# Kernel optimization log

Hardware: AMD Instinct MI355X
Metric: run time of the kernel (lower is better)

The kernel has to match this reference:

```python
import jax, jax.numpy as jnp
import numpy as np

LATENT_D = 32      # latent_dim
MAX_TRIES = 10     # max_tries_sampling
EPS = 1e-40

def _conv(x, W, b, stride, pad):
    y = jax.lax.conv_general_dilated(x, W, (stride, stride), [(pad, pad), (pad, pad)],
                                     dimension_numbers=('NCHW', 'OIHW', 'NCHW'))
    return y + b[None, :, None, None]

def _normalize(v, axis=-1):
    n = jnp.sqrt(jnp.clip(jnp.sum(v * v, axis=axis, keepdims=True), 1e-24))
    return v / n

def wood_sample_vMF(mu, kappa, key):
    # mu: [B,d] unit vectors, kappa: [B]
    B, d = mu.shape
    alpha = d - 1.0
    k_w, k_v = jax.random.split(key)

    def body(i, carry):
        w, acc = carry
        k1 = jax.random.fold_in(k_w, 2 * i)
        k2 = jax.random.fold_in(k_w, 2 * i + 1)
        w_cand = 2.0 * jax.random.uniform(k1, (B,)) - 1.0
        one_minus_w2 = jnp.clip(1.0 - w_cand * w_cand, EPS)
        log_p = kappa * w_cand + 0.5 * (alpha - 2.0) * jnp.log(one_minus_w2)
        log_r = jnp.log(jax.random.uniform(k2, (B,)) + EPS)
        newly = (log_r + kappa <= log_p) & (~acc)
        w = jnp.where(newly, w_cand, w)
        return w, acc | newly

    w, _ = jax.lax.fori_loop(0, MAX_TRIES, body,
                             (jnp.zeros((B,)), jnp.zeros((B,), dtype=bool)))
    w = jnp.clip(w, -1.0, 1.0)
    v = _normalize(jax.random.normal(k_v, (B, d - 1)))      # tangent direction
    sqrt_term = jnp.sqrt(jnp.clip(1.0 - w * w, EPS))
    z_tilde = jnp.concatenate([sqrt_term[:, None] * v, w[:, None]], axis=1)  # [B,d]
    e_d = jnp.zeros((d,)).at[-1].set(1.0)
    u = _normalize(e_d[None, :] - mu)                        # Householder axis
    dot_val = jnp.sum(z_tilde * u, axis=-1, keepdims=True)
    return z_tilde - 2.0 * dot_val * u

def setup_inputs() -> dict:
    key = jax.random.key(0)
    ks = jax.random.split(key, 16)
    B = 64
    s = 0.05
    inp = {
        'x':   jax.random.normal(ks[0], (B, 6, 224, 224), jnp.float32),
        # stand-in resnet encoder (resnet_out_dim=512)
        'W1':  jax.random.normal(ks[1], (64, 6, 7, 7)) * s,   'b1': jnp.zeros((64,)),
        'W2':  jax.random.normal(ks[2], (256, 64, 3, 3)) * s, 'b2': jnp.zeros((256,)),
        'Wh':  jax.random.normal(ks[3], (256, 512)) * s,      'bh': jnp.zeros((512,)),
        # vMF heads
        'Wmu': jax.random.normal(ks[4], (512, LATENT_D)) * s, 'bmu': jnp.zeros((LATENT_D,)),
        'Wk':  jax.random.normal(ks[5], (512, 1)) * s,        'bk': jnp.zeros((1,)),
        # ResNetMLP(32 -> 512 -> 512 -> 32 -> 7)
        'M1': jax.random.normal(ks[6], (LATENT_D, 512)) * s,  'bM1': jnp.zeros((512,)),
        'M2': jax.random.normal(ks[7], (512, 512)) * s,       'bM2': jnp.zeros((512,)),
        'M3': jax.random.normal(ks[8], (512, 32)) * s,        'bM3': jnp.zeros((32,)),
        'M4': jax.random.normal(ks[9], (32, 7)) * s,          'bM4': jnp.zeros((7,)),
    }
    return inp

def reference(x, W1, b1, W2, b2, Wh, bh, Wmu, bmu, Wk, bk,
              M1, bM1, M2, bM2, M3, bM3, M4, bM4):
    # encoder: conv stack -> global avg pool -> fc (resnet_out_dim=512)
    h = jax.nn.relu(_conv(x, W1, b1, stride=4, pad=3))   # [B,64,56,56]
    h = jax.nn.relu(_conv(h, W2, b2, stride=2, pad=1))   # [B,256,28,28]
    h = jnp.mean(h, axis=(2, 3))                         # [B,256]
    h = h @ Wh + bh                                      # [B,512]
    mu = _normalize(h @ Wmu + bmu)                       # [B,32] on sphere
    kappa = jax.nn.softplus(h @ Wk + bk) + 1.0           # [B,1]
    z = wood_sample_vMF(mu, kappa[:, 0], jax.random.key(42))
    # MLP head
    y = jax.nn.relu(z @ M1 + bM1)
    y = jax.nn.relu(y @ M2 + bM2)
    y = jax.nn.relu(y @ M3 + bM3)
    out = y @ M4 + bM4                                   # [B,7]
    return out, mu, kappa
```

## Files before the change

### kernel.cpp

```cpp
#include <hip/hip_runtime.h>
#include <hip/hip_bf16.h>
#include <cstdint>

__device__ __forceinline__ uint32_t rotl32(uint32_t v, int n) {
    return (v << n) | (v >> (32 - n));
}

__device__ __forceinline__ void threefry2x32(uint32_t k0, uint32_t k1,
                                             uint32_t x0, uint32_t x1,
                                             uint32_t& o0, uint32_t& o1) {
    uint32_t ks2 = 0x1BD11BDAu ^ k0 ^ k1;
    uint32_t v0 = x0 + k0, v1 = x1 + k1;
    v0 += v1; v1 = rotl32(v1, 13); v1 ^= v0;
    v0 += v1; v1 = rotl32(v1, 15); v1 ^= v0;
    v0 += v1; v1 = rotl32(v1, 26); v1 ^= v0;
    v0 += v1; v1 = rotl32(v1, 6);  v1 ^= v0;
    v0 += k1; v1 += ks2 + 1u;
    v0 += v1; v1 = rotl32(v1, 17); v1 ^= v0;
    v0 += v1; v1 = rotl32(v1, 29); v1 ^= v0;
    v0 += v1; v1 = rotl32(v1, 16); v1 ^= v0;
    v0 += v1; v1 = rotl32(v1, 24); v1 ^= v0;
    v0 += ks2; v1 += k0 + 2u;
    v0 += v1; v1 = rotl32(v1, 13); v1 ^= v0;
    v0 += v1; v1 = rotl32(v1, 15); v1 ^= v0;
    v0 += v1; v1 = rotl32(v1, 26); v1 ^= v0;
    v0 += v1; v1 = rotl32(v1, 6);  v1 ^= v0;
    v0 += k0; v1 += k1 + 3u;
    v0 += v1; v1 = rotl32(v1, 17); v1 ^= v0;
    v0 += v1; v1 = rotl32(v1, 29); v1 ^= v0;
    v0 += v1; v1 = rotl32(v1, 16); v1 ^= v0;
    v0 += v1; v1 = rotl32(v1, 24); v1 ^= v0;
    v0 += k1; v1 += ks2 + 4u;
    v0 += v1; v1 = rotl32(v1, 13); v1 ^= v0;
    v0 += v1; v1 = rotl32(v1, 15); v1 ^= v0;
    v0 += v1; v1 = rotl32(v1, 26); v1 ^= v0;
    v0 += v1; v1 = rotl32(v1, 6);  v1 ^= v0;
    v0 += ks2; v1 += k0 + 5u;
    o0 = v0; o1 = v1;
}

__device__ __forceinline__ float bits_to_unit_float(uint32_t bits) {
    return __uint_as_float((bits >> 9) | 0x3F800000u) - 1.0f;
}

__device__ __forceinline__ float erfinv_f(float x) {
    float w = -log1pf(-x * x);
    float p;
    if (w < 5.0f) {
        w = w - 2.5f;
        p = 2.81022636e-08f;
        p = fmaf(p, w, 3.43273939e-07f);
        p = fmaf(p, w, -3.5233877e-06f);
        p = fmaf(p, w, -4.39150654e-06f);
        p = fmaf(p, w, 0.00021858087f);
        p = fmaf(p, w, -0.00125372503f);
        p = fmaf(p, w, -0.00417768164f);
        p = fmaf(p, w, 0.246640727f);
        p = fmaf(p, w, 1.50140941f);
    } else {
        w = sqrtf(w) - 3.0f;
        p = -0.000200214257f;
        p = fmaf(p, w, 0.000100950558f);
        p = fmaf(p, w, 0.00134934322f);
        p = fmaf(p, w, -0.00367342844f);
        p = fmaf(p, w, 0.00573950773f);
        p = fmaf(p, w, -0.0076224613f);
        p = fmaf(p, w, 0.00943887047f);
        p = fmaf(p, w, 1.00167406f);
        p = fmaf(p, w, 2.83297682f);
    }
    return p * x;
}

__global__ __launch_bounds__(256) void transpose_W2(const float* __restrict__ W2,
                                                    float* __restrict__ W2T) {
    __shared__ float t[32][33];
    int pT = blockIdx.x % 18;
    int oT = blockIdx.x / 18;
    int c = threadIdx.x & 31, r8 = threadIdx.x >> 5;
    #pragma unroll
    for (int rr = 0; rr < 4; ++rr) {
        int oc = oT * 32 + r8 + 8 * rr;
        t[r8 + 8 * rr][c] = W2[oc * 576 + pT * 32 + c];
    }
    __syncthreads();
    #pragma unroll
    for (int rr = 0; rr < 4; ++rr) {
        int p = pT * 32 + r8 + 8 * rr;
        W2T[p * 256 + oT * 32 + c] = t[c][r8 + 8 * rr];
    }
}

__global__ __launch_bounds__(256) void conv1_tiled(const float* __restrict__ x,
                                                   const float* __restrict__ W1,
                                                   const float* __restrict__ b1,
                                                   float* __restrict__ out) {
    int bid = blockIdx.x;
    int ocT = bid & 1;
    int ohT = (bid >> 1) % 7;
    int b   = bid / 14;
    int tid = threadIdx.x;
    int ocg = tid & 3;
    int owg = (tid >> 2) & 7;
    int ohh = tid >> 5;

    __shared__ __align__(16) float w1s[294 * 32];
    for (int idx = tid; idx < 9408; idx += 256) {
        int p = idx >> 5, ocl = idx & 31;
        w1s[idx] = W1[(ocT * 32 + ocl) * 294 + p];
    }
    __syncthreads();

    int oh = ohT * 8 + ohh;
    int iwst = 28 * owg - 4;
    const float* xb = x + (size_t)b * 6 * 50176;

    float acc[8][7] = {};

    #pragma unroll 1
    for (int ic = 0; ic < 6; ++ic) {
        #pragma unroll 1
        for (int kh = 0; kh < 7; ++kh) {
            int ih = 4 * oh - 3 + kh;
            if ((unsigned)ih >= 224u) continue;
            const float* xrow = xb + ic * 50176 + ih * 224 + iwst;
            float r[32];
            {
                float2 v0 = (owg > 0) ? *reinterpret_cast<const float2*>(xrow)
                                      : make_float2(0.0f, 0.0f);
                float2 v1 = (owg > 0) ? *reinterpret_cast<const float2*>(xrow + 2)
                                      : make_float2(0.0f, 0.0f);
                r[0] = v0.x; r[1] = v0.y; r[2] = v1.x; r[3] = v1.y;
            }
            #pragma unroll
            for (int t = 2; t < 16; ++t) {
                float2 v2 = *reinterpret_cast<const float2*>(xrow + 2 * t);
                r[2 * t] = v2.x; r[2 * t + 1] = v2.y;
            }
            const float* wp = &w1s[(ic * 49 + kh * 7) * 32 + 8 * ocg];
            #pragma unroll
            for (int kw = 0; kw < 7; ++kw) {
                float4 wa = *reinterpret_cast<const float4*>(wp + kw * 32);
                float4 wb = *reinterpret_cast<const float4*>(wp + kw * 32 + 4);
                #pragma unroll
                for (int j = 0; j < 7; ++j) {
                    float xv = r[4 * j + kw + 1];
                    acc[0][j] = fmaf(xv, wa.x, acc[0][j]);
                    acc[1][j] = fmaf(xv, wa.y, acc[1][j]);
                    acc[2][j] = fmaf(xv, wa.z, acc[2][j]);
                    acc[3][j] = fmaf(xv, wa.w, acc[3][j]);
                    acc[4][j] = fmaf(xv, wb.x, acc[4][j]);
                    acc[5][j] = fmaf(xv, wb.y, acc[5][j]);
                    acc[6][j] = fmaf(xv, wb.z, acc[6][j]);
                    acc[7][j] = fmaf(xv, wb.w, acc[7][j]);
                }
            }
        }
    }

    int oc0 = ocT * 32 + 8 * ocg;
    #pragma unroll
    for (int q = 0; q < 8; ++q) {
        float bias = b1[oc0 + q];
        float* orow = out + (((size_t)b * 64 + oc0 + q) * 56 + oh) * 56 + 7 * owg;
        #pragma unroll
        for (int j = 0; j < 7; ++j) orow[j] = fmaxf(acc[q][j] + bias, 0.0f);
    }
}

__global__ __launch_bounds__(256) void conv2_tiled(const float* __restrict__ c1,
                                                   const float* __restrict__ W2T,
                                                   const float* __restrict__ b2,
                                                   float* __restrict__ part2) {
    int bid = blockIdx.x;
    int ocT = bid & 1;
    int ohT = (bid >> 1) % 7;
    int b   = bid / 14;
    int tid = threadIdx.x;
    int ocg = tid & 15;
    int owg = (tid >> 4) & 3;
    int ohh = tid >> 6;

    __shared__ __align__(16) float w2s[72 * 128];
    float* red = w2s;

    int oh = 4 * ohT + ohh;
    int start = 14 * owg - 2;

    float acc[8][7] = {};

    #pragma unroll 1
    for (int chunk = 0; chunk < 8; ++chunk) {
        int ic0 = chunk * 8;
        __syncthreads();
        for (int idx = tid; idx < 9216; idx += 256) {
            int pl = idx >> 7, ocl = idx & 127;
            w2s[idx] = W2T[((size_t)(ic0 * 9 + pl)) * 256 + ocT * 128 + ocl];
        }
        __syncthreads();

        #pragma unroll 1
        for (int icl = 0; icl < 8; ++icl) {
            const float* crow0 = c1 + (((size_t)b * 64 + ic0 + icl) * 56) * 56;
            #pragma unroll 1
            for (int kh = 0; kh < 3; ++kh) {
                int ih = 2 * oh - 1 + kh;
                if ((unsigned)ih >= 56u) continue;
                const float* xrow = crow0 + ih * 56 + start;
                float r[16];
                {
                    float2 v0 = (owg > 0) ? *reinterpret_cast<const float2*>(xrow)
                                          : make_float2(0.0f, 0.0f);
                    r[0] = v0.x; r[1] = v0.y;
                }
                #pragma unroll
                for (int t = 1; t < 8; ++t) {
                    float2 v2 = *reinterpret_cast<const float2*>(xrow + 2 * t);
                    r[2 * t] = v2.x; r[2 * t + 1] = v2.y;
                }
                int pb = icl * 9 + kh * 3;
                #pragma unroll
                for (int kw = 0; kw < 3; ++kw) {
                    float4 wa = *reinterpret_cast<const float4*>(&w2s[(pb + kw) * 128 + 4 * ocg]);
                    float4 wb = *reinterpret_cast<const float4*>(&w2s[(pb + kw) * 128 + 64 + 4 * ocg]);
                    #pragma unroll
                    for (int j = 0; j < 7; ++j) {
                        float xv = r[2 * j + kw + 1];
                        acc[0][j] = fmaf(xv, wa.x, acc[0][j]);
                        acc[1][j] = fmaf(xv, wa.y, acc[1][j]);
                        acc[2][j] = fmaf(xv, wa.z, acc[2][j]);
                        acc[3][j] = fmaf(xv, wa.w, acc[3][j]);
                        acc[4][j] = fmaf(xv, wb.x, acc[4][j]);
                        acc[5][j] = fmaf(xv, wb.y, acc[5][j]);
                        acc[6][j] = fmaf(xv, wb.z, acc[6][j]);
                        acc[7][j] = fmaf(xv, wb.w, acc[7][j]);
                    }
                }
            }
        }
    }

    __syncthreads();
    int sp = ohh * 4 + owg;
    #pragma unroll
    for (int q = 0; q < 8; ++q) {
        int ocl = (q < 4) ? (ocg * 4 + q) : (64 + ocg * 4 + (q - 4));
        float bias = b2[ocT * 128 + ocl];
        float s = 0.0f;
        #pragma unroll
        for (int j = 0; j < 7; ++j) s += fmaxf(acc[q][j] + bias, 0.0f);
        red[ocl * 16 + sp] = s;
    }
    __syncthreads();
    if (tid < 128) {
        float s = 0.0f;
        #pragma unroll
        for (int i = 0; i < 16; ++i) s += red[tid * 16 + i];
        part2[((size_t)ohT * 64 + b) * 256 + ocT * 128 + tid] = s;
    }
}

__global__ __launch_bounds__(512) void head_fused(const float* __restrict__ part2,
                                                  const float* __restrict__ Wh,
                                                  const float* __restrict__ bh,
                                                  const float* __restrict__ Wmu,
                                                  const float* __restrict__ bmu,
                                                  const float* __restrict__ Wk,
                                                  const float* __restrict__ bk,
                                                  float* __restrict__ out) {
    int b = blockIdx.x, tid = threadIdx.x;
    __shared__ float ps[256], hs[512], ms[32], red2[512], kred[16];
    __shared__ float nrm;
    if (tid < 256) {
        float s = 0.0f;
        #pragma unroll
        for (int t = 0; t < 7; ++t) s += part2[((size_t)t * 64 + b) * 256 + tid];
        ps[tid] = s * (1.0f / 784.0f);
    }
    __syncthreads();
    {
        float acc = bh[tid];
        for (int i = 0; i < 256; ++i) acc = fmaf(ps[i], Wh[i * 512 + tid], acc);
        hs[tid] = acc;
    }
    __syncthreads();
    {
        int m = tid >> 4, part = tid & 15;
        int j0 = part * 32;
        float acc = 0.0f;
        #pragma unroll
        for (int jj = 0; jj < 32; ++jj) acc = fmaf(hs[j0 + jj], Wmu[(j0 + jj) * 32 + m], acc);
        red2[m * 16 + part] = acc;
    }
    if (tid < 16) {
        int j0 = tid * 32;
        float acc = 0.0f;
        #pragma unroll
        for (int jj = 0; jj < 32; ++jj) acc = fmaf(hs[j0 + jj], Wk[j0 + jj], acc);
        kred[tid] = acc;
    }
    __syncthreads();
    if (tid < 32) {
        float acc = bmu[tid];
        #pragma unroll
        for (int p = 0; p < 16; ++p) acc += red2[tid * 16 + p];
        ms[tid] = acc;
    }
    if (tid == 32) {
        float acc = bk[0];
        #pragma unroll
        for (int p = 0; p < 16; ++p) acc += kred[p];
        float sp = fmaxf(acc, 0.0f) + log1pf(expf(-fabsf(acc)));
        out[2496 + b] = sp + 1.0f;
    }
    __syncthreads();
    if (tid == 0) {
        float ss = 0.0f;
        for (int k = 0; k < 32; ++k) ss += ms[k] * ms[k];
        nrm = sqrtf(fmaxf(ss, 1e-24f));
    }
    __syncthreads();
    if (tid < 32) out[448 + b * 32 + tid] = ms[tid] / nrm;
}

__global__ __launch_bounds__(512) void mlp_head(const float* __restrict__ M1, const float* __restrict__ bM1,
                                                const float* __restrict__ M2, const float* __restrict__ bM2,
                                                const float* __restrict__ M3, const float* __restrict__ bM3,
                                                const float* __restrict__ M4, const float* __restrict__ bM4,
                                                float* __restrict__ out) {
    int b = blockIdx.x;
    int tid = threadIdx.x;
    __shared__ float vsh[31], wcs[10], zsh[32], y1[512], y2[512], y3[32];
    __shared__ int accs[10];

    if (tid < 31) {
        uint32_t y00, y01, y10, y11;
        threefry2x32(0u, 42u, 0u, 2u, y00, y01);
        threefry2x32(0u, 42u, 1u, 3u, y10, y11);
        uint32_t kv0 = y01, kv1 = y11;
        int idx = b * 31 + tid;
        int word = (idx >= 992);
        uint32_t pp = (uint32_t)(word ? idx - 992 : idx);
        uint32_t a0, a1;
        threefry2x32(kv0, kv1, pp, 992u + pp, a0, a1);
        uint32_t bits = word ? a1 : a0;
        float f = bits_to_unit_float(bits);
        const float LO = -0.99999994f;
        float u = fmaxf(LO, f * 2.0f + LO);
        vsh[tid] = 1.41421356f * erfinv_f(u);
    } else if (tid >= 64 && tid < 74) {
        uint32_t y00, y01, y10, y11;
        threefry2x32(0u, 42u, 0u, 2u, y00, y01);
        threefry2x32(0u, 42u, 1u, 3u, y10, y11);
        uint32_t kw0 = y00, kw1 = y10;
        int i = tid - 64;
        float kappa = out[2496 + b];
        uint32_t k10, k11, k20, k21, z0, z1;
        threefry2x32(kw0, kw1, 0u, (uint32_t)(2 * i), k10, k11);
        threefry2x32(kw0, kw1, 0u, (uint32_t)(2 * i + 1), k20, k21);
        uint32_t p = (uint32_t)(b & 31);
        threefry2x32(k10, k11, p, 32u + p, z0, z1);
        uint32_t bits = (b < 32) ? z0 : z1;
        float u1 = bits_to_unit_float(bits);
        float wc = 2.0f * u1 - 1.0f;
        float om = fmaxf(1.0f - wc * wc, 1e-40f);
        float logp = kappa * wc + 14.5f * logf(om);
        threefry2x32(k20, k21, p, 32u + p, z0, z1);
        bits = (b < 32) ? z0 : z1;
        float logr = logf(bits_to_unit_float(bits) + 1e-40f);
        wcs[i] = wc;
        accs[i] = (logr + kappa <= logp) ? 1 : 0;
    }
    __syncthreads();
    if (tid == 0) {
        float w = 0.0f;
        bool acc = false;
        #pragma unroll
        for (int i = 0; i < 10; ++i) {
            bool newly = (accs[i] != 0) && !acc;
            if (newly) w = wcs[i];
            acc = acc || newly;
        }
        w = fminf(fmaxf(w, -1.0f), 1.0f);
        float ss = 0.0f;
        #pragma unroll
        for (int j = 0; j < 31; ++j) ss += vsh[j] * vsh[j];
        float vinv = 1.0f / sqrtf(fmaxf(ss, 1e-24f));
        float st = sqrtf(fmaxf(1.0f - w * w, 1e-40f));
        float zt[32];
        #pragma unroll
        for (int j = 0; j < 31; ++j) zt[j] = st * (vsh[j] * vinv);
        zt[31] = w;
        float uv[32];
        float us = 0.0f;
        #pragma unroll
        for (int k = 0; k < 32; ++k) {
            float m = out[448 + b * 32 + k];
            float e = (k == 31) ? 1.0f : 0.0f;
            float t = e - m;
            uv[k] = t;
            us += t * t;
        }
        float un = sqrtf(fmaxf(us, 1e-24f));
        float dot = 0.0f;
        #pragma unroll
        for (int k = 0; k < 32; ++k) {
            uv[k] = uv[k] / un;
            dot += zt[k] * uv[k];
        }
        #pragma unroll
        for (int k = 0; k < 32; ++k) zsh[k] = zt[k] - 2.0f * dot * uv[k];
    }
    __syncthreads();

    float acc = bM1[tid];
    #pragma unroll
    for (int k = 0; k < 32; k++) acc = fmaf(zsh[k], M1[k * 512 + tid], acc);
    y1[tid] = fmaxf(acc, 0.0f);
    __syncthreads();
    acc = bM2[tid];
    for (int k = 0; k < 512; k++) acc = fmaf(y1[k], M2[k * 512 + tid], acc);
    y2[tid] = fmaxf(acc, 0.0f);
    __syncthreads();
    if (tid < 32) {
        acc = bM3[tid];
        for (int k = 0; k < 512; k++) acc = fmaf(y2[k], M3[k * 32 + tid], acc);
        y3[tid] = fmaxf(acc, 0.0f);
    }
    __syncthreads();
    if (tid < 7) {
        acc = bM4[tid];
        #pragma unroll
        for (int k = 0; k < 32; k++) acc = fmaf(y3[k], M4[k * 7 + tid], acc);
        out[b * 7 + tid] = acc;
    }
}

extern "C" void kernel_launch(void* const* d_in, const int* in_sizes, int n_in,
                              void* d_out, int out_size, void* d_ws, size_t ws_size,
                              hipStream_t stream) {
    const float* x   = (const float*)d_in[0];
    const float* W1  = (const float*)d_in[1];
    const float* b1  = (const float*)d_in[2];
    const float* W2  = (const float*)d_in[3];
    const float* b2  = (const float*)d_in[4];
    const float* Wh  = (const float*)d_in[5];
    const float* bh  = (const float*)d_in[6];
    const float* Wmu = (const float*)d_in[7];
    const float* bmu = (const float*)d_in[8];
    const float* Wk  = (const float*)d_in[9];
    const float* bk  = (const float*)d_in[10];
    const float* M1  = (const float*)d_in[11];
    const float* bM1 = (const float*)d_in[12];
    const float* M2  = (const float*)d_in[13];
    const float* bM2 = (const float*)d_in[14];
    const float* M3  = (const float*)d_in[15];
    const float* bM3 = (const float*)d_in[16];
    const float* M4  = (const float*)d_in[17];
    const float* bM4 = (const float*)d_in[18];

    float* out = (float*)d_out;
    float* ws  = (float*)d_ws;

    float* W2T   = ws;
    float* c1    = W2T + 147456;
    float* part2 = c1 + 12845056;

    transpose_W2<<<144, 256, 0, stream>>>(W2, W2T);
    conv1_tiled<<<896, 256, 0, stream>>>(x, W1, b1, c1);
    conv2_tiled<<<896, 256, 0, stream>>>(c1, W2T, b2, part2);
    head_fused<<<64, 512, 0, stream>>>(part2, Wh, bh, Wmu, bmu, Wk, bk, out);
    mlp_head<<<64, 512, 0, stream>>>(M1, bM1, M2, bM2, M3, bM3, M4, bM4, out);
}
```

Measured before the change: 446.7 us.

## Double-buffer conv2 input rows and vectorize weight staging loads

Restructures the conv2 inner loop to prefetch the next input row into a second register buffer while computing FMAs on the current one. Out-of-range top rows now read from a zeroed scratch row instead of branching, so the loop is fully unrolled per pair of channels. Weight staging into shared memory uses float4 loads. This raises register pressure and adds a zero-row write in the transpose kernel.

Measured after the change: 546.1 us. +22.3%, slower.

```diff
diff --git a/kernel.cpp b/kernel.cpp
--- a/kernel.cpp
+++ b/kernel.cpp
@@ -73,7 +73,9 @@
 }
 
 __global__ __launch_bounds__(256) void transpose_W2(const float* __restrict__ W2,
-                                                    float* __restrict__ W2T) {
+                                                    float* __restrict__ W2T,
+                                                    float* __restrict__ zrow) {
+    if (blockIdx.x == 0 && threadIdx.x < 128) zrow[threadIdx.x] = 0.0f;
     __shared__ float t[32][33];
     int pT = blockIdx.x % 18;
     int oT = blockIdx.x / 18;
@@ -168,9 +170,47 @@
     }
 }
 
+
+#define LOADROW(R, KH, CH) do {                                                        \
+    int ih_ = 2 * oh - 1 + (KH);                                                       \
+    const float* xr_ = (ih_ >= 0)                                                      \
+        ? (c1 + ((size_t)(b * 64) + (CH)) * 3136 + ih_ * 56 + start)                   \
+        : (zrow + start);                                                              \
+    float2 v0_ = (owg > 0) ? *reinterpret_cast<const float2*>(xr_)                     \
+                           : make_float2(0.0f, 0.0f);                                  \
+    R[0] = v0_.x; R[1] = v0_.y;                                                        \
+    _Pragma("unroll")                                                                  \
+    for (int t_ = 1; t_ < 8; ++t_) {                                                   \
+        float2 v_ = *reinterpret_cast<const float2*>(xr_ + 2 * t_);                    \
+        R[2 * t_] = v_.x; R[2 * t_ + 1] = v_.y;                                        \
+    }                                                                                  \
+} while (0)
+
+#define FMASTAGE(R, ICL, KH) do {                                                      \
+    int pb_ = (ICL) * 9 + (KH) * 3;                                                    \
+    _Pragma("unroll")                                                                  \
+    for (int kw = 0; kw < 3; ++kw) {                                                   \
+        float4 wa = *reinterpret_cast<const float4*>(&w2s[(pb_ + kw) * 128 + 4 * ocg]);\
+        float4 wb = *reinterpret_cast<const float4*>(&w2s[(pb_ + kw) * 128 + 64 + 4 * ocg]);\
+        _Pragma("unroll")                                                              \
+        for (int j = 0; j < 7; ++j) {                                                  \
+            float xv = R[2 * j + kw + 1];                                              \
+            acc[0][j] = fmaf(xv, wa.x, acc[0][j]);                                     \
+            acc[1][j] = fmaf(xv, wa.y, acc[1][j]);                                     \
+            acc[2][j] = fmaf(xv, wa.z, acc[2][j]);                                     \
+            acc[3][j] = fmaf(xv, wa.w, acc[3][j]);                                     \
+            acc[4][j] = fmaf(xv, wb.x, acc[4][j]);                                     \
+            acc[5][j] = fmaf(xv, wb.y, acc[5][j]);                                     \
+            acc[6][j] = fmaf(xv, wb.z, acc[6][j]);                                     \
+            acc[7][j] = fmaf(xv, wb.w, acc[7][j]);                                     \
+        }                                                                              \
+    }                                                                                  \
+} while (0)
+
 __global__ __launch_bounds__(256) void conv2_tiled(const float* __restrict__ c1,
                                                    const float* __restrict__ W2T,
                                                    const float* __restrict__ b2,
+                                                   const float* __restrict__ zrow,
                                                    float* __restrict__ part2) {
     int bid = blockIdx.x;
     int ocT = bid & 1;
@@ -188,55 +228,31 @@
     int start = 14 * owg - 2;
 
     float acc[8][7] = {};
+    float rA[16], rB[16];
+
+    LOADROW(rA, 0, 0);
 
     #pragma unroll 1
     for (int chunk = 0; chunk < 8; ++chunk) {
         int ic0 = chunk * 8;
         __syncthreads();
-        for (int idx = tid; idx < 9216; idx += 256) {
-            int pl = idx >> 7, ocl = idx & 127;
-            w2s[idx] = W2T[((size_t)(ic0 * 9 + pl)) * 256 + ocT * 128 + ocl];
+        for (int idx4 = tid; idx4 < 2304; idx4 += 256) {
+            int pl = idx4 >> 5, o4 = idx4 & 31;
+            *reinterpret_cast<float4*>(&w2s[pl * 128 + o4 * 4]) =
+                *reinterpret_cast<const float4*>(&W2T[((size_t)(ic0 * 9 + pl)) * 256 + ocT * 128 + o4 * 4]);
         }
         __syncthreads();
 
         #pragma unroll 1
-        for (int icl = 0; icl < 8; ++icl) {
-            const float* crow0 = c1 + (((size_t)b * 64 + ic0 + icl) * 56) * 56;
-            #pragma unroll 1
-            for (int kh = 0; kh < 3; ++kh) {
-                int ih = 2 * oh - 1 + kh;
-                if ((unsigned)ih >= 56u) continue;
-                const float* xrow = crow0 + ih * 56 + start;
-                float r[16];
-                {
-                    float2 v0 = (owg > 0) ? *reinterpret_cast<const float2*>(xrow)
-                                          : make_float2(0.0f, 0.0f);
-                    r[0] = v0.x; r[1] = v0.y;
-                }
-                #pragma unroll
-                for (int t = 1; t < 8; ++t) {
-                    float2 v2 = *reinterpret_cast<const float2*>(xrow + 2 * t);
-                    r[2 * t] = v2.x; r[2 * t + 1] = v2.y;
-                }
-                int pb = icl * 9 + kh * 3;
-                #pragma unroll
-                for (int kw = 0; kw < 3; ++kw) {
-                    float4 wa = *reinterpret_cast<const float4*>(&w2s[(pb + kw) * 128 + 4 * ocg]);
-                    float4 wb = *reinterpret_cast<const float4*>(&w2s[(pb + kw) * 128 + 64 + 4 * ocg]);
-                    #pragma unroll
-                    for (int j = 0; j < 7; ++j) {
-                        float xv = r[2 * j + kw + 1];
-                        acc[0][j] = fmaf(xv, wa.x, acc[0][j]);
-                        acc[1][j] = fmaf(xv, wa.y, acc[1][j]);
-                        acc[2][j] = fmaf(xv, wa.z, acc[2][j]);
-                        acc[3][j] = fmaf(xv, wa.w, acc[3][j]);
-                        acc[4][j] = fmaf(xv, wb.x, acc[4][j]);
-                        acc[5][j] = fmaf(xv, wb.y, acc[5][j]);
-                        acc[6][j] = fmaf(xv, wb.z, acc[6][j]);
-                        acc[7][j] = fmaf(xv, wb.w, acc[7][j]);
-                    }
-                }
-            }
+        for (int icl = 0; icl < 8; icl += 2) {
+            int ch = ic0 + icl;
+            LOADROW(rB, 1, ch);       FMASTAGE(rA, icl, 0);
+            LOADROW(rA, 2, ch);       FMASTAGE(rB, icl, 1);
+            LOADROW(rB, 0, ch + 1);   FMASTAGE(rA, icl, 2);
+            LOADROW(rA, 1, ch + 1);   FMASTAGE(rB, icl + 1, 0);
+            LOADROW(rB, 2, ch + 1);   FMASTAGE(rA, icl + 1, 1);
+            int nch = min(ch + 2, 63);
+            LOADROW(rA, 0, nch);      FMASTAGE(rB, icl + 1, 2);
         }
     }
 
@@ -465,10 +481,11 @@
     float* W2T   = ws;
     float* c1    = W2T + 147456;
     float* part2 = c1 + 12845056;
-
-    transpose_W2<<<144, 256, 0, stream>>>(W2, W2T);
+    float* zrow  = part2 + 114688;
+
+    transpose_W2<<<144, 256, 0, stream>>>(W2, W2T, zrow);
     conv1_tiled<<<896, 256, 0, stream>>>(x, W1, b1, c1);
-    conv2_tiled<<<896, 256, 0, stream>>>(c1, W2T, b2, part2);
+    conv2_tiled<<<896, 256, 0, stream>>>(c1, W2T, b2, zrow, part2);
     head_fused<<<64, 512, 0, stream>>>(part2, Wh, bh, Wmu, bmu, Wk, bk, out);
     mlp_head<<<64, 512, 0, stream>>>(M1, bM1, M2, bM2, M3, bM3, M4, bM4, out);
 }
```

## Split conv2 input channels across blocks and add combine kernel

Applied to the files above, without the earlier changes.

Conv2 now runs on twice as many blocks, each handling half of the input channels with a smaller shared-memory weight tile. Weight staging uses float4 loads. Each block writes its raw per-position partial sums to a large workspace, and a new combine kernel adds the two halves, applies bias and ReLU, and pools. This aims to raise occupancy and parallelism, at the cost of a large extra global memory write and read plus an additional kernel launch.

After: 417.7 us. 6.5% less time.

```diff
diff --git a/kernel.cpp b/kernel.cpp
--- a/kernel.cpp
+++ b/kernel.cpp
@@ -173,15 +173,16 @@
                                                    const float* __restrict__ b2,
                                                    float* __restrict__ part2) {
     int bid = blockIdx.x;
-    int ocT = bid & 1;
-    int ohT = (bid >> 1) % 7;
-    int b   = bid / 14;
+    int icT = bid & 1;
+    int ocT = (bid >> 1) & 1;
+    int ohT = (bid >> 2) % 7;
+    int b   = bid / 28;
     int tid = threadIdx.x;
     int ocg = tid & 15;
     int owg = (tid >> 4) & 3;
     int ohh = tid >> 6;
 
-    __shared__ __align__(16) float w2s[72 * 128];
+    __shared__ __align__(16) float w2s[36 * 128];
     float* red = w2s;
 
     int oh = 4 * ohT + ohh;
@@ -191,16 +192,17 @@
 
     #pragma unroll 1
     for (int chunk = 0; chunk < 8; ++chunk) {
-        int ic0 = chunk * 8;
+        int ic0 = icT * 32 + chunk * 4;
         __syncthreads();
-        for (int idx = tid; idx < 9216; idx += 256) {
-            int pl = idx >> 7, ocl = idx & 127;
-            w2s[idx] = W2T[((size_t)(ic0 * 9 + pl)) * 256 + ocT * 128 + ocl];
+        for (int idx4 = tid; idx4 < 1152; idx4 += 256) {
+            int pl = idx4 >> 5, o4 = idx4 & 31;
+            *reinterpret_cast<float4*>(&w2s[pl * 128 + o4 * 4]) =
+                *reinterpret_cast<const float4*>(&W2T[((size_t)(ic0 * 9 + pl)) * 256 + ocT * 128 + o4 * 4]);
         }
         __syncthreads();
 
         #pragma unroll 1
-        for (int icl = 0; icl < 8; ++icl) {
+        for (int icl = 0; icl < 4; ++icl) {
             const float* crow0 = c1 + (((size_t)b * 64 + ic0 + icl) * 56) * 56;
             #pragma unroll 1
             for (int kh = 0; kh < 3; ++kh) {
@@ -245,19 +247,53 @@
     #pragma unroll
     for (int q = 0; q < 8; ++q) {
         int ocl = (q < 4) ? (ocg * 4 + q) : (64 + ocg * 4 + (q - 4));
-        float bias = b2[ocT * 128 + ocl];
         float s = 0.0f;
         #pragma unroll
-        for (int j = 0; j < 7; ++j) s += fmaxf(acc[q][j] + bias, 0.0f);
-        red[ocl * 16 + sp] = s;
-    }
-    __syncthreads();
-    if (tid < 128) {
-        float s = 0.0f;
-        #pragma unroll
-        for (int i = 0; i < 16; ++i) s += red[tid * 16 + i];
-        part2[((size_t)ohT * 64 + b) * 256 + ocT * 128 + tid] = s;
-    }
+        for (int j = 0; j < 7; ++j) s += acc[q][j];
+        (void)s;
+    }
+    {
+        float* px = part2 +
+            ((((size_t)icT * 64 + b) * 7 + ohT) * 2 + ocT) * (128 * 16 * 7);
+        #pragma unroll
+        for (int q = 0; q < 8; ++q) {
+            int ocl = (q < 4) ? (ocg * 4 + q) : (64 + ocg * 4 + (q - 4));
+            #pragma unroll
+            for (int j = 0; j < 7; ++j)
+                px[(ocl * 16 + sp) * 7 + j] = acc[q][j];
+        }
+    }
+}
+
+__global__ __launch_bounds__(256) void conv2_combine(const float* __restrict__ px_all,
+                                                     const float* __restrict__ b2,
+                                                     float* __restrict__ pooled_part) {
+    int bid = blockIdx.x;
+    int ocT = bid & 1;
+    int ohT = (bid >> 1) % 7;
+    int b   = bid / 14;
+    int tid = threadIdx.x;
+    int ocl = tid >> 1;
+    int hh  = tid & 1;
+
+    const float* px0 = px_all + ((((size_t)0 * 64 + b) * 7 + ohT) * 2 + ocT) * (128 * 16 * 7);
+    const float* px1 = px_all + ((((size_t)1 * 64 + b) * 7 + ohT) * 2 + ocT) * (128 * 16 * 7);
+    float bias = b2[ocT * 128 + ocl];
+    float s = 0.0f;
+    #pragma unroll
+    for (int spl = 0; spl < 8; ++spl) {
+        int sp = hh * 8 + spl;
+        #pragma unroll
+        for (int j = 0; j < 7; ++j) {
+            float v = px0[(ocl * 16 + sp) * 7 + j] + px1[(ocl * 16 + sp) * 7 + j] + bias;
+            s += fmaxf(v, 0.0f);
+        }
+    }
+    __shared__ float red[256];
+    red[tid] = s;
+    __syncthreads();
+    if (hh == 0)
+        pooled_part[(((size_t)ohT * 64 + b) * 256) + ocT * 128 + ocl] = red[tid] + red[tid + 1];
 }
 
 __global__ __launch_bounds__(512) void head_fused(const float* __restrict__ part2,
@@ -462,13 +498,15 @@
     float* out = (float*)d_out;
     float* ws  = (float*)d_ws;
 
-    float* W2T   = ws;
-    float* c1    = W2T + 147456;
-    float* part2 = c1 + 12845056;
+    float* W2T     = ws;
+    float* c1      = W2T + 147456;
+    float* px      = c1 + 12845056;
+    float* pooledp = px + 25690112;
 
     transpose_W2<<<144, 256, 0, stream>>>(W2, W2T);
     conv1_tiled<<<896, 256, 0, stream>>>(x, W1, b1, c1);
-    conv2_tiled<<<896, 256, 0, stream>>>(c1, W2T, b2, part2);
-    head_fused<<<64, 512, 0, stream>>>(part2, Wh, bh, Wmu, bmu, Wk, bk, out);
+    conv2_tiled<<<1792, 256, 0, stream>>>(c1, W2T, b2, px);
+    conv2_combine<<<896, 256, 0, stream>>>(px, b2, pooledp);
+    head_fused<<<64, 512, 0, stream>>>(pooledp, Wh, bh, Wmu, bmu, Wk, bk, out);
     mlp_head<<<64, 512, 0, stream>>>(M1, bM1, M2, bM2, M3, bM3, M4, bM4, out);
 }
```
